# Performance work log

Hardware: AMD Instinct MI355X
Metric: run time of the kernel (lower is better)

Reference implementation:

```python
import jax, jax.numpy as jnp
import numpy as np

T = 4096   # total packed tokens
NQ = 16    # query heads
NK = 4     # kv heads (GQA)
HN = 128   # head dim


def setup_inputs() -> dict:
    key = jax.random.key(0)
    kq, kk, kv = jax.random.split(key, 3)
    return {
        "query": jax.random.normal(kq, (T, NQ, HN), dtype=jnp.float32),
        "key": jax.random.normal(kk, (T, NK, HN), dtype=jnp.float32),
        "value": jax.random.normal(kv, (T, NK, HN), dtype=jnp.float32),
        # packed varlen boundaries (4 sequences)
        "cu_seqlens": jnp.array([0, 1536, 2048, 3584, 4096], dtype=jnp.int32),
    }


def reference(query, key, value, cu_seqlens):
    t, nq, hn = query.shape
    nk = key.shape[1]
    rep = nq // nk  # GQA expansion factor
    scale = hn ** -0.5
    # [h, t, d] layout (matches torch unsqueeze(0).permute(0,2,1,3), batch=1)
    q = jnp.transpose(query, (1, 0, 2))
    k = jnp.repeat(jnp.transpose(key, (1, 0, 2)), rep, axis=0)
    v = jnp.repeat(jnp.transpose(value, (1, 0, 2)), rep, axis=0)
    # full scores [h, t, t]
    scores = jnp.einsum('hqd,hkd->hqk', q, k) * scale
    # block-diagonal causal mask from cu_seqlens
    idx = jnp.arange(t)
    seg = jnp.searchsorted(cu_seqlens[1:], idx, side='right')  # segment id per token
    allowed = (seg[:, None] == seg[None, :]) & (idx[None, :] <= idx[:, None])
    scores = jnp.where(allowed[None, :, :], scores, -jnp.inf)
    p = jax.nn.softmax(scores, axis=-1)  # every row keeps its diagonal -> no NaN
    out = jnp.einsum('hqk,hkd->hqd', p, v)
    # [t, nq*hn]
    return jnp.transpose(out, (1, 0, 2)).reshape(t, nq * hn)
```

## Files before the change

kernel.cpp:

```cpp
#include <hip/hip_runtime.h>
#include <hip/hip_bf16.h>
#include <cstdint>
#include <cstddef>

#define NQH 16
#define NKH 4
#define HN 128
#define QBLK 64
#define KBLK 64
#define QSCALE 0.12751589542585458f

typedef __bf16 bf16x8 __attribute__((ext_vector_type(8)));
typedef float f32x4 __attribute__((ext_vector_type(4)));

__device__ __forceinline__ void gload16(const void* g, void* l) {
  __builtin_amdgcn_global_load_lds(
      (const __attribute__((address_space(1))) void*)g,
      (__attribute__((address_space(3))) void*)l, 16, 0, 0);
}

__global__ __launch_bounds__(256) void cvt_k(const float* __restrict__ K,
                                             __bf16* __restrict__ Kb, int T) {
  const size_t idx8 = ((size_t)blockIdx.x * 256 + threadIdx.x) * 8;
  const int d = (int)(idx8 & 127);
  const int kvh = (int)((idx8 >> 7) & 3);
  const size_t t = idx8 >> 9;
  float4 a = *(const float4*)&K[idx8];
  float4 b = *(const float4*)&K[idx8 + 4];
  bf16x8 f;
  f[0] = (__bf16)a.x; f[1] = (__bf16)a.y; f[2] = (__bf16)a.z; f[3] = (__bf16)a.w;
  f[4] = (__bf16)b.x; f[5] = (__bf16)b.y; f[6] = (__bf16)b.z; f[7] = (__bf16)b.w;
  *(bf16x8*)&Kb[(size_t)kvh * T * HN + t * HN + d] = f;
}

__global__ __launch_bounds__(128) void cvt_v(const float* __restrict__ V,
                                             __bf16* __restrict__ Vb, int T) {
  const int d = threadIdx.x;
  const int t0 = blockIdx.x * 8;
  const int kvh = blockIdx.y;
  bf16x8 f;
#pragma unroll
  for (int i = 0; i < 8; ++i)
    f[i] = (__bf16)V[(size_t)(t0 + i) * (NKH * HN) + kvh * HN + d];
  *(bf16x8*)&Vb[(size_t)kvh * HN * T + (size_t)d * T + t0] = f;
}

template <bool MASKED>
__device__ __forceinline__ void attn_iter(
    const char* Kc, const char* Vc, const bf16x8 qfA[4], const bf16x8 qfB[4],
    int ln, int hi, int limA, float& mA, float& lA, f32x4* accA,
    float& mB, float& lB, f32x4* accB) {
  f32x4 sA[4], sB[4];
#pragma unroll
  for (int c = 0; c < 4; ++c) {
    sA[c] = (f32x4){0.f, 0.f, 0.f, 0.f};
    sB[c] = (f32x4){0.f, 0.f, 0.f, 0.f};
  }
  __builtin_amdgcn_s_setprio(1);
#pragma unroll
  for (int kc = 0; kc < 4; ++kc) {
#pragma unroll
    for (int c = 0; c < 4; ++c) {
      const int row = c * 16 + ln;
      const bf16x8 kf =
          *(const bf16x8*)(Kc + row * 256 + (((kc * 4 + hi) ^ (row & 7)) << 4));
      sA[c] = __builtin_amdgcn_mfma_f32_16x16x32_bf16(kf, qfA[kc], sA[c], 0, 0, 0);
      sB[c] = __builtin_amdgcn_mfma_f32_16x16x32_bf16(kf, qfB[kc], sB[c], 0, 0, 0);
    }
  }
  __builtin_amdgcn_s_setprio(0);

  if (MASKED) {
    const int limB = limA + 16;
#pragma unroll
    for (int c = 0; c < 4; ++c)
#pragma unroll
      for (int i = 0; i < 4; ++i) {
        const int koff = ((c >> 1) << 5) + hi * 8 + ((c & 1) << 2) + i;
        sA[c][i] = (koff <= limA) ? sA[c][i] : -1e30f;
        sB[c][i] = (koff <= limB) ? sB[c][i] : -1e30f;
      }
  }

  float mmA = fmaxf(
      fmaxf(fmaxf(fmaxf(sA[0][0], sA[0][1]), fmaxf(sA[0][2], sA[0][3])),
            fmaxf(fmaxf(sA[1][0], sA[1][1]), fmaxf(sA[1][2], sA[1][3]))),
      fmaxf(fmaxf(fmaxf(sA[2][0], sA[2][1]), fmaxf(sA[2][2], sA[2][3])),
            fmaxf(fmaxf(sA[3][0], sA[3][1]), fmaxf(sA[3][2], sA[3][3]))));
  float mmB = fmaxf(
      fmaxf(fmaxf(fmaxf(sB[0][0], sB[0][1]), fmaxf(sB[0][2], sB[0][3])),
            fmaxf(fmaxf(sB[1][0], sB[1][1]), fmaxf(sB[1][2], sB[1][3]))),
      fmaxf(fmaxf(fmaxf(sB[2][0], sB[2][1]), fmaxf(sB[2][2], sB[2][3])),
            fmaxf(fmaxf(sB[3][0], sB[3][1]), fmaxf(sB[3][2], sB[3][3]))));
  mmA = fmaxf(mmA, __shfl_xor(mmA, 16));
  mmA = fmaxf(mmA, __shfl_xor(mmA, 32));
  mmB = fmaxf(mmB, __shfl_xor(mmB, 16));
  mmB = fmaxf(mmB, __shfl_xor(mmB, 32));

  if (__any((mmA > mA + 8.0f) | (mmB > mB + 8.0f))) {
    const float mnA = fmaxf(mA, mmA), mnB = fmaxf(mB, mmB);
    const float cA = exp2f(mA - mnA), cB = exp2f(mB - mnB);
    mA = mnA; mB = mnB;
    lA *= cA; lB *= cB;
#pragma unroll
    for (int dt = 0; dt < 8; ++dt) { accA[dt] *= cA; accB[dt] *= cB; }
  }

  float pA[4][4], pB[4][4];
  float psA = 0.f, psB = 0.f;
#pragma unroll
  for (int c = 0; c < 4; ++c)
#pragma unroll
    for (int i = 0; i < 4; ++i) {
      pA[c][i] = exp2f(sA[c][i] - mA); psA += pA[c][i];
      pB[c][i] = exp2f(sB[c][i] - mB); psB += pB[c][i];
    }
  psA += __shfl_xor(psA, 16); psA += __shfl_xor(psA, 32);
  psB += __shfl_xor(psB, 16); psB += __shfl_xor(psB, 32);
  lA += psA; lB += psB;

  bf16x8 paA[2], paB[2];
#pragma unroll
  for (int ch = 0; ch < 2; ++ch)
#pragma unroll
    for (int e = 0; e < 8; ++e) {
      paA[ch][e] = (__bf16)pA[2 * ch + (e >> 2)][e & 3];
      paB[ch][e] = (__bf16)pB[2 * ch + (e >> 2)][e & 3];
    }

  __builtin_amdgcn_s_setprio(1);
#pragma unroll
  for (int ch = 0; ch < 2; ++ch) {
#pragma unroll
    for (int dt = 0; dt < 8; ++dt) {
      const int vr = dt * 16 + ln;
      const bf16x8 vb =
          *(const bf16x8*)(Vc + vr * 128 + (((ch * 4 + hi) ^ (vr & 7)) << 4));
      accA[dt] = __builtin_amdgcn_mfma_f32_16x16x32_bf16(vb, paA[ch], accA[dt], 0, 0, 0);
      accB[dt] = __builtin_amdgcn_mfma_f32_16x16x32_bf16(vb, paB[ch], accB[dt], 0, 0, 0);
    }
  }
  __builtin_amdgcn_s_setprio(0);
}

__global__ __launch_bounds__(256, 2) void attn_mfma9(
    const float* __restrict__ Q, const __bf16* __restrict__ Kb,
    const __bf16* __restrict__ Vb, const int* __restrict__ cu,
    float* __restrict__ O, int T, int nseg) {
  const int tid = threadIdx.x;
  const int w = tid >> 6, lane = tid & 63;
  const int g = w >> 1, wv = w & 1;
  const int ln = lane & 15, hi = lane >> 4;
  const int h = blockIdx.x & 15;
  const int my_rank = blockIdx.x >> 4;
  const int kvh = h >> 2;

  __shared__ __bf16 K_lds[2][KBLK * HN];
  __shared__ __bf16 V_lds[2][HN * KBLK];
  __shared__ float ml1[QBLK][2];
  __shared__ int s_tile;

  if (w == 0) {
    const int t2 = lane;
    const int r0t = t2 << 6;
    int st = 0;
    for (int s = 1; s < nseg; ++s) { const int c = cu[s]; if (c <= r0t) st = c; }
    const int dep = r0t + QBLK - st;
    int rk = 0;
    for (int j = 0; j < 64; ++j) {
      const int dj = __shfl(dep, j);
      rk += (dj > dep) || (dj == dep && j < t2);
    }
    if (rk == my_rank) s_tile = t2;
  }
  __syncthreads();
  const int r0 = s_tile << 6;

  int st0 = 0;
  for (int s = 1; s < nseg; ++s) { const int c = cu[s]; if (c <= r0) st0 = c; }
  const int kstart = st0;
  const int nloc = (r0 + QBLK - kstart) >> 6;
  const int n0 = (nloc + 1) >> 1;
  const int myn = g ? (nloc - n0) : n0;
  const int gbeg = kstart + (g ? n0 * KBLK : 0);

  const __bf16* KbH = Kb + (size_t)kvh * T * HN;
  const __bf16* VbH = Vb + (size_t)kvh * HN * T;

  bf16x8 qfA[4], qfB[4];
  {
    const float* qpA = &Q[(size_t)(r0 + wv * 32 + ln) * (NQH * HN) + h * HN];
    const float* qpB = qpA + (size_t)16 * (NQH * HN);
#pragma unroll
    for (int kc = 0; kc < 4; ++kc) {
      float4 a0 = *(const float4*)(qpA + kc * 32 + hi * 8);
      float4 a1 = *(const float4*)(qpA + kc * 32 + hi * 8 + 4);
      float4 b0 = *(const float4*)(qpB + kc * 32 + hi * 8);
      float4 b1 = *(const float4*)(qpB + kc * 32 + hi * 8 + 4);
      bf16x8 fa, fb;
      fa[0] = (__bf16)(a0.x * QSCALE); fa[1] = (__bf16)(a0.y * QSCALE);
      fa[2] = (__bf16)(a0.z * QSCALE); fa[3] = (__bf16)(a0.w * QSCALE);
      fa[4] = (__bf16)(a1.x * QSCALE); fa[5] = (__bf16)(a1.y * QSCALE);
      fa[6] = (__bf16)(a1.z * QSCALE); fa[7] = (__bf16)(a1.w * QSCALE);
      fb[0] = (__bf16)(b0.x * QSCALE); fb[1] = (__bf16)(b0.y * QSCALE);
      fb[2] = (__bf16)(b0.z * QSCALE); fb[3] = (__bf16)(b0.w * QSCALE);
      fb[4] = (__bf16)(b1.x * QSCALE); fb[5] = (__bf16)(b1.y * QSCALE);
      fb[6] = (__bf16)(b1.z * QSCALE); fb[7] = (__bf16)(b1.w * QSCALE);
      qfA[kc] = fa; qfB[kc] = fb;
    }
  }

  float mA = 0.f, lA = 0.f, mB = 0.f, lB = 0.f;
  f32x4 accA[8], accB[8];
#pragma unroll
  for (int dt = 0; dt < 8; ++dt) {
    accA[dt] = (f32x4){0.f, 0.f, 0.f, 0.f};
    accB[dt] = (f32x4){0.f, 0.f, 0.f, 0.f};
  }

  const int gl = wv * 64 + lane;
  const int slK = gl & 15;
  const int Rb = gl >> 4;
  const int kcol = ((slK ^ (Rb & 7)) << 3);
  const int svV = gl & 7;
  const int db = gl >> 3;
  const int vcol = ((svV ^ (db & 7)) << 3);
  char* ldsK = (char*)&K_lds[g][0] + (size_t)gl * 16;
  char* ldsV = (char*)&V_lds[g][0] + (size_t)gl * 16;

  const int relA = wv * 32 + ln;
  const char* Kc = (const char*)&K_lds[g][0];
  const char* Vc = (const char*)&V_lds[g][0];

  for (int it = 0; it < n0; ++it) {
    const bool act = (it < myn);
    const int kb = gbeg + it * KBLK;
    if (act) {
#pragma unroll
      for (int j = 0; j < 8; ++j) {
        const int R = Rb + 8 * j;
        const int c = R >> 4, r = R & 15;
        const int keyoff = ((c >> 1) << 5) + ((r >> 2) << 3) + ((c & 1) << 2) + (r & 3);
        gload16(KbH + (size_t)(kb + keyoff) * HN + kcol, ldsK + j * 2048);
      }
#pragma unroll
      for (int j = 0; j < 8; ++j)
        gload16(VbH + (size_t)(db + 16 * j) * T + kb + vcol, ldsV + j * 2048);
    }
    __syncthreads();
    if (act) {
      if (kb >= r0)
        attn_iter<true>(Kc, Vc, qfA, qfB, ln, hi, relA - (kb - r0), mA, lA,
                        accA, mB, lB, accB);
      else
        attn_iter<false>(Kc, Vc, qfA, qfB, ln, hi, 0, mA, lA, accA, mB, lB, accB);
    }
    __syncthreads();
  }

  float* accf = (float*)&K_lds[0][0];
  if (g == 1) {
    if (hi == 0) {
      ml1[relA][0] = mA;      ml1[relA][1] = lA;
      ml1[relA + 16][0] = mB; ml1[relA + 16][1] = lB;
    }
#pragma unroll
    for (int dt = 0; dt < 8; ++dt) {
      *(f32x4*)&accf[relA * 128 + ((dt ^ (relA & 7)) << 4) + (hi << 2)] = accA[dt];
      *(f32x4*)&accf[(relA + 16) * 128 + ((dt ^ ((relA + 16) & 7)) << 4) + (hi << 2)] = accB[dt];
    }
  }
  __syncthreads();
  if (g == 0) {
#pragma unroll
    for (int set = 0; set < 2; ++set) {
      const int row = relA + set * 16;
      const float mg = set ? mB : mA;
      const float lg = set ? lB : lA;
      f32x4* acc = set ? accB : accA;
      const float m1 = ml1[row][0], l1v = ml1[row][1];
      float c0 = 1.f, c1 = 0.f, l = lg;
      if (l1v != 0.f) {
        const float m = fmaxf(mg, m1);
        c0 = exp2f(mg - m); c1 = exp2f(m1 - m);
        l = lg * c0 + l1v * c1;
      }
      const float inv = 1.0f / l;
      float* op = &O[(size_t)(r0 + row) * (NQH * HN) + h * HN];
#pragma unroll
      for (int dt = 0; dt < 8; ++dt) {
        const f32x4 a1 = *(const f32x4*)&accf[row * 128 + ((dt ^ (row & 7)) << 4) + (hi << 2)];
        const f32x4 res = (acc[dt] * c0 + a1 * c1) * inv;
        *(f32x4*)&op[dt * 16 + hi * 4] = res;
      }
    }
  }
}

extern "C" void kernel_launch(void* const* d_in, const int* in_sizes, int n_in,
                              void* d_out, int out_size, void* d_ws, size_t ws_size,
                              hipStream_t stream) {
  const float* Q = (const float*)d_in[0];
  const float* K = (const float*)d_in[1];
  const float* V = (const float*)d_in[2];
  const int* cu = (const int*)d_in[3];
  float* O = (float*)d_out;

  const int T = in_sizes[0] / (NQH * HN);
  const int nseg = in_sizes[3] - 1;

  const size_t need = (size_t)2 * NKH * T * HN * sizeof(__bf16);
  if (ws_size < need) return;

  __bf16* Kb = (__bf16*)d_ws;
  __bf16* Vb = (__bf16*)d_ws + (size_t)NKH * T * HN;

  const int nelem = T * NKH * HN;
  cvt_k<<<nelem / 8 / 256, 256, 0, stream>>>(K, Kb, T);
  cvt_v<<<dim3(T / 8, NKH), 128, 0, stream>>>(V, Vb, T);

  attn_mfma9<<<1024, 256, 0, stream>>>(Q, Kb, Vb, cu, O, T, nseg);
}
```

Before: 69.36 us.

## Halve key block to 32, raise occupancy, and snake-order block scheduling

Shrinks the key/value tile from 64 to 32 keys. This halves LDS use (one shared byte buffer) and the per-iteration score registers, so the launch bound asks for 4 blocks per CU instead of 2. The split-K between the two wave groups becomes an even split of 32-key blocks, which removes the idle inactive iterations, and the LDS swizzles are re-derived for the new tile shapes. Block IDs are remapped in a serpentine order across rounds of 256 to balance heavy and light tiles. In exchange there are twice as many barriers and load rounds per key, with less MFMA work between syncs.

```diff
diff --git a/kernel.cpp b/kernel.cpp
--- a/kernel.cpp
+++ b/kernel.cpp
@@ -7,7 +7,7 @@
 #define NKH 4
 #define HN 128
 #define QBLK 64
-#define KBLK 64
+#define KBLK 32
 #define QSCALE 0.12751589542585458f
 
 typedef __bf16 bf16x8 __attribute__((ext_vector_type(8)));
@@ -48,11 +48,11 @@
 template <bool MASKED>
 __device__ __forceinline__ void attn_iter(
     const char* Kc, const char* Vc, const bf16x8 qfA[4], const bf16x8 qfB[4],
-    int ln, int hi, int limA, float& mA, float& lA, f32x4* accA,
+    int ln, int hi, int vslot, int limA, float& mA, float& lA, f32x4* accA,
     float& mB, float& lB, f32x4* accB) {
-  f32x4 sA[4], sB[4];
-#pragma unroll
-  for (int c = 0; c < 4; ++c) {
+  f32x4 sA[2], sB[2];
+#pragma unroll
+  for (int c = 0; c < 2; ++c) {
     sA[c] = (f32x4){0.f, 0.f, 0.f, 0.f};
     sB[c] = (f32x4){0.f, 0.f, 0.f, 0.f};
   }
@@ -60,10 +60,10 @@
 #pragma unroll
   for (int kc = 0; kc < 4; ++kc) {
 #pragma unroll
-    for (int c = 0; c < 4; ++c) {
+    for (int c = 0; c < 2; ++c) {
       const int row = c * 16 + ln;
       const bf16x8 kf =
-          *(const bf16x8*)(Kc + row * 256 + (((kc * 4 + hi) ^ (row & 7)) << 4));
+          *(const bf16x8*)(Kc + row * 256 + (((kc * 4 + hi) ^ (ln & 7)) << 4));
       sA[c] = __builtin_amdgcn_mfma_f32_16x16x32_bf16(kf, qfA[kc], sA[c], 0, 0, 0);
       sB[c] = __builtin_amdgcn_mfma_f32_16x16x32_bf16(kf, qfB[kc], sB[c], 0, 0, 0);
     }
@@ -73,25 +73,19 @@
   if (MASKED) {
     const int limB = limA + 16;
 #pragma unroll
-    for (int c = 0; c < 4; ++c)
+    for (int c = 0; c < 2; ++c)
 #pragma unroll
       for (int i = 0; i < 4; ++i) {
-        const int koff = ((c >> 1) << 5) + hi * 8 + ((c & 1) << 2) + i;
+        const int koff = hi * 8 + c * 4 + i;
         sA[c][i] = (koff <= limA) ? sA[c][i] : -1e30f;
         sB[c][i] = (koff <= limB) ? sB[c][i] : -1e30f;
       }
   }
 
-  float mmA = fmaxf(
-      fmaxf(fmaxf(fmaxf(sA[0][0], sA[0][1]), fmaxf(sA[0][2], sA[0][3])),
-            fmaxf(fmaxf(sA[1][0], sA[1][1]), fmaxf(sA[1][2], sA[1][3]))),
-      fmaxf(fmaxf(fmaxf(sA[2][0], sA[2][1]), fmaxf(sA[2][2], sA[2][3])),
-            fmaxf(fmaxf(sA[3][0], sA[3][1]), fmaxf(sA[3][2], sA[3][3]))));
-  float mmB = fmaxf(
-      fmaxf(fmaxf(fmaxf(sB[0][0], sB[0][1]), fmaxf(sB[0][2], sB[0][3])),
-            fmaxf(fmaxf(sB[1][0], sB[1][1]), fmaxf(sB[1][2], sB[1][3]))),
-      fmaxf(fmaxf(fmaxf(sB[2][0], sB[2][1]), fmaxf(sB[2][2], sB[2][3])),
-            fmaxf(fmaxf(sB[3][0], sB[3][1]), fmaxf(sB[3][2], sB[3][3]))));
+  float mmA = fmaxf(fmaxf(fmaxf(sA[0][0], sA[0][1]), fmaxf(sA[0][2], sA[0][3])),
+                    fmaxf(fmaxf(sA[1][0], sA[1][1]), fmaxf(sA[1][2], sA[1][3])));
+  float mmB = fmaxf(fmaxf(fmaxf(sB[0][0], sB[0][1]), fmaxf(sB[0][2], sB[0][3])),
+                    fmaxf(fmaxf(sB[1][0], sB[1][1]), fmaxf(sB[1][2], sB[1][3])));
   mmA = fmaxf(mmA, __shfl_xor(mmA, 16));
   mmA = fmaxf(mmA, __shfl_xor(mmA, 32));
   mmB = fmaxf(mmB, __shfl_xor(mmB, 16));
@@ -106,10 +100,10 @@
     for (int dt = 0; dt < 8; ++dt) { accA[dt] *= cA; accB[dt] *= cB; }
   }
 
-  float pA[4][4], pB[4][4];
+  float pA[2][4], pB[2][4];
   float psA = 0.f, psB = 0.f;
 #pragma unroll
-  for (int c = 0; c < 4; ++c)
+  for (int c = 0; c < 2; ++c)
 #pragma unroll
     for (int i = 0; i < 4; ++i) {
       pA[c][i] = exp2f(sA[c][i] - mA); psA += pA[c][i];
@@ -119,31 +113,25 @@
   psB += __shfl_xor(psB, 16); psB += __shfl_xor(psB, 32);
   lA += psA; lB += psB;
 
-  bf16x8 paA[2], paB[2];
-#pragma unroll
-  for (int ch = 0; ch < 2; ++ch)
-#pragma unroll
-    for (int e = 0; e < 8; ++e) {
-      paA[ch][e] = (__bf16)pA[2 * ch + (e >> 2)][e & 3];
-      paB[ch][e] = (__bf16)pB[2 * ch + (e >> 2)][e & 3];
-    }
+  bf16x8 paA, paB;
+#pragma unroll
+  for (int e = 0; e < 8; ++e) {
+    paA[e] = (__bf16)pA[e >> 2][e & 3];
+    paB[e] = (__bf16)pB[e >> 2][e & 3];
+  }
 
   __builtin_amdgcn_s_setprio(1);
 #pragma unroll
-  for (int ch = 0; ch < 2; ++ch) {
-#pragma unroll
-    for (int dt = 0; dt < 8; ++dt) {
-      const int vr = dt * 16 + ln;
-      const bf16x8 vb =
-          *(const bf16x8*)(Vc + vr * 128 + (((ch * 4 + hi) ^ (vr & 7)) << 4));
-      accA[dt] = __builtin_amdgcn_mfma_f32_16x16x32_bf16(vb, paA[ch], accA[dt], 0, 0, 0);
-      accB[dt] = __builtin_amdgcn_mfma_f32_16x16x32_bf16(vb, paB[ch], accB[dt], 0, 0, 0);
-    }
+  for (int dt = 0; dt < 8; ++dt) {
+    const int vr = dt * 16 + ln;
+    const bf16x8 vb = *(const bf16x8*)(Vc + vr * 64 + vslot);
+    accA[dt] = __builtin_amdgcn_mfma_f32_16x16x32_bf16(vb, paA, accA[dt], 0, 0, 0);
+    accB[dt] = __builtin_amdgcn_mfma_f32_16x16x32_bf16(vb, paB, accB[dt], 0, 0, 0);
   }
   __builtin_amdgcn_s_setprio(0);
 }
 
-__global__ __launch_bounds__(256, 2) void attn_mfma9(
+__global__ __launch_bounds__(256, 4) void attn_mfma10(
     const float* __restrict__ Q, const __bf16* __restrict__ Kb,
     const __bf16* __restrict__ Vb, const int* __restrict__ cu,
     float* __restrict__ O, int T, int nseg) {
@@ -151,14 +139,17 @@
   const int w = tid >> 6, lane = tid & 63;
   const int g = w >> 1, wv = w & 1;
   const int ln = lane & 15, hi = lane >> 4;
-  const int h = blockIdx.x & 15;
-  const int my_rank = blockIdx.x >> 4;
+
+  const int bid = blockIdx.x;
+  const int round = bid >> 8, pos = bid & 255;
+  const int rr = (round & 1) ? ((round << 8) | (255 - pos)) : bid;
+  const int h = rr & 15;
+  const int my_rank = rr >> 4;
   const int kvh = h >> 2;
 
-  __shared__ __bf16 K_lds[2][KBLK * HN];
-  __shared__ __bf16 V_lds[2][HN * KBLK];
-  __shared__ float ml1[QBLK][2];
-  __shared__ int s_tile;
+  __shared__ __align__(16) char smem[33296];
+  float* ml1 = (float*)(smem + 32768);
+  int* s_tile = (int*)(smem + 33280);
 
   if (w == 0) {
     const int t2 = lane;
@@ -171,18 +162,16 @@
       const int dj = __shfl(dep, j);
       rk += (dj > dep) || (dj == dep && j < t2);
     }
-    if (rk == my_rank) s_tile = t2;
+    if (rk == my_rank) *s_tile = t2;
   }
   __syncthreads();
-  const int r0 = s_tile << 6;
+  const int r0 = *s_tile << 6;
 
   int st0 = 0;
   for (int s = 1; s < nseg; ++s) { const int c = cu[s]; if (c <= r0) st0 = c; }
   const int kstart = st0;
-  const int nloc = (r0 + QBLK - kstart) >> 6;
-  const int n0 = (nloc + 1) >> 1;
-  const int myn = g ? (nloc - n0) : n0;
-  const int gbeg = kstart + (g ? n0 * KBLK : 0);
+  const int n0 = (r0 + QBLK - kstart) >> 6;
+  const int gbeg = kstart + g * n0 * KBLK;
 
   const __bf16* KbH = Kb + (size_t)kvh * T * HN;
   const __bf16* VbH = Vb + (size_t)kvh * HN * T;
@@ -219,50 +208,46 @@
   }
 
   const int gl = wv * 64 + lane;
-  const int slK = gl & 15;
-  const int Rb = gl >> 4;
-  const int kcol = ((slK ^ (Rb & 7)) << 3);
-  const int svV = gl & 7;
-  const int db = gl >> 3;
-  const int vcol = ((svV ^ (db & 7)) << 3);
-  char* ldsK = (char*)&K_lds[g][0] + (size_t)gl * 16;
-  char* ldsV = (char*)&V_lds[g][0] + (size_t)gl * 16;
-
+  const int Rb = gl >> 4, sK = gl & 15;
+  int key_j[4];
+#pragma unroll
+  for (int j = 0; j < 4; ++j)
+    key_j[j] = ((Rb >> 2) << 3) + (Rb & 3) + ((j & 1) << 4) + ((j >> 1) << 2);
+  const int kcolE = ((sK ^ Rb) << 3);
+  const int db = gl >> 2, sV = gl & 3;
+  const int swz_d = (db & 3) ^ ((db >> 2) & 3);
+  const int vkeyE = ((sV ^ swz_d) << 3);
+  char* ldsK = smem + g * 8192 + (size_t)gl * 16;
+  char* ldsV = smem + 16384 + g * 8192 + (size_t)gl * 16;
+  const int vslot = ((hi ^ (ln & 3) ^ ((ln >> 2) & 3)) << 4);
+
+  const char* Kc = smem + g * 8192;
+  const char* Vc = smem + 16384 + g * 8192;
   const int relA = wv * 32 + ln;
-  const char* Kc = (const char*)&K_lds[g][0];
-  const char* Vc = (const char*)&V_lds[g][0];
 
   for (int it = 0; it < n0; ++it) {
-    const bool act = (it < myn);
     const int kb = gbeg + it * KBLK;
-    if (act) {
-#pragma unroll
-      for (int j = 0; j < 8; ++j) {
-        const int R = Rb + 8 * j;
-        const int c = R >> 4, r = R & 15;
-        const int keyoff = ((c >> 1) << 5) + ((r >> 2) << 3) + ((c & 1) << 2) + (r & 3);
-        gload16(KbH + (size_t)(kb + keyoff) * HN + kcol, ldsK + j * 2048);
-      }
-#pragma unroll
-      for (int j = 0; j < 8; ++j)
-        gload16(VbH + (size_t)(db + 16 * j) * T + kb + vcol, ldsV + j * 2048);
-    }
+#pragma unroll
+    for (int j = 0; j < 4; ++j)
+      gload16(KbH + (size_t)(kb + key_j[j]) * HN + kcolE, ldsK + j * 2048);
+#pragma unroll
+    for (int j = 0; j < 4; ++j)
+      gload16(VbH + (size_t)(db + 32 * j) * T + kb + vkeyE, ldsV + j * 2048);
     __syncthreads();
-    if (act) {
-      if (kb >= r0)
-        attn_iter<true>(Kc, Vc, qfA, qfB, ln, hi, relA - (kb - r0), mA, lA,
-                        accA, mB, lB, accB);
-      else
-        attn_iter<false>(Kc, Vc, qfA, qfB, ln, hi, 0, mA, lA, accA, mB, lB, accB);
-    }
+    if (kb >= r0)
+      attn_iter<true>(Kc, Vc, qfA, qfB, ln, hi, vslot, relA - (kb - r0), mA,
+                      lA, accA, mB, lB, accB);
+    else
+      attn_iter<false>(Kc, Vc, qfA, qfB, ln, hi, vslot, 0, mA, lA, accA, mB,
+                       lB, accB);
     __syncthreads();
   }
 
-  float* accf = (float*)&K_lds[0][0];
+  float* accf = (float*)smem;
   if (g == 1) {
     if (hi == 0) {
-      ml1[relA][0] = mA;      ml1[relA][1] = lA;
-      ml1[relA + 16][0] = mB; ml1[relA + 16][1] = lB;
+      ml1[relA * 2] = mA;            ml1[relA * 2 + 1] = lA;
+      ml1[(relA + 16) * 2] = mB;     ml1[(relA + 16) * 2 + 1] = lB;
     }
 #pragma unroll
     for (int dt = 0; dt < 8; ++dt) {
@@ -278,7 +263,7 @@
       const float mg = set ? mB : mA;
       const float lg = set ? lB : lA;
       f32x4* acc = set ? accB : accA;
-      const float m1 = ml1[row][0], l1v = ml1[row][1];
+      const float m1 = ml1[row * 2], l1v = ml1[row * 2 + 1];
       float c0 = 1.f, c1 = 0.f, l = lg;
       if (l1v != 0.f) {
         const float m = fmaxf(mg, m1);
@@ -319,5 +304,5 @@
   cvt_k<<<nelem / 8 / 256, 256, 0, stream>>>(K, Kb, T);
   cvt_v<<<dim3(T / 8, NKH), 128, 0, stream>>>(V, Vb, T);
 
-  attn_mfma9<<<1024, 256, 0, stream>>>(Q, Kb, Vb, cu, O, T, nseg);
-}
+  attn_mfma10<<<1024, 256, 0, stream>>>(Q, Kb, Vb, cu, O, T, nseg);
+}
```

Measured after the change: 161.1 us. 2.32x slower.
